# Optimization experiments

Hardware: AMD Instinct MI355X
Metric: run time of the kernel (lower is better)

The kernel has to match this reference:

```python
import jax, jax.numpy as jnp
import numpy as np

N_NODES = 100000
N_EDGES = 3200000
F_IN = 128
HID = 64
N_GRAPHS = 256
N_CLASSES = 8


def setup_inputs() -> dict:
    key = jax.random.key(0)
    ks = jax.random.split(key, 8)
    x = jax.random.normal(ks[0], (N_NODES, F_IN), dtype=jnp.float32)
    edge_index = jax.random.randint(ks[1], (2, N_EDGES), 0, N_NODES, dtype=jnp.int64)
    batch = jnp.sort(jax.random.randint(ks[2], (N_NODES,), 0, N_GRAPHS, dtype=jnp.int64))
    def glorot(k, fan_in, fan_out):
        s = np.sqrt(6.0 / (fan_in + fan_out)).astype(np.float32)
        return jax.random.uniform(k, (fan_in, fan_out), jnp.float32, -s, s)
    return {
        "x": x,
        "edge_index": edge_index,
        "batch": batch,
        "W1": glorot(ks[3], F_IN, HID),
        "b1": jnp.zeros((HID,), jnp.float32),
        "W2": glorot(ks[4], HID, HID),
        "b2": jnp.zeros((HID,), jnp.float32),
        "Wf1": glorot(ks[5], HID, 32),
        "bf1": jnp.zeros((32,), jnp.float32),
        "Wf2": glorot(ks[6], 32, N_CLASSES),
        "bf2": jnp.zeros((N_CLASSES,), jnp.float32),
    }


def gcn_conv(x, src, dst, dis, W, b, num_nodes):
    # PyG GCNConv: x' = D^{-1/2} (A + I) D^{-1/2} (x W) + b
    xw = x @ W  # [N, out]
    norm = dis[src] * dis[dst]  # [E+N] per-edge symmetric normalization
    out = jax.ops.segment_sum(norm[:, None] * xw[src], dst, num_segments=num_nodes)
    return out + b


def reference(x, edge_index, batch, W1, b1, W2, b2, Wf1, bf1, Wf2, bf2):
    n = x.shape[0]
    loop = jnp.arange(n, dtype=edge_index.dtype)
    src = jnp.concatenate([edge_index[0], loop])  # add self-loops (PyG default)
    dst = jnp.concatenate([edge_index[1], loop])
    deg = jax.ops.segment_sum(jnp.ones_like(dst, dtype=x.dtype), dst, num_segments=n)
    dis = jnp.where(deg > 0, jax.lax.rsqrt(jnp.maximum(deg, 1.0)), 0.0)

    h = jax.nn.relu(gcn_conv(x, src, dst, dis, W1, b1, n))
    h = gcn_conv(h, src, dst, dis, W2, b2, n)

    # global_mean_pool over graph segment ids
    sums = jax.ops.segment_sum(h, batch, num_segments=N_GRAPHS)  # [G, 64]
    counts = jax.ops.segment_sum(jnp.ones((n,), h.dtype), batch, num_segments=N_GRAPHS)
    pooled = sums / jnp.maximum(counts, 1.0)[:, None]

    out = jax.nn.relu(pooled @ Wf1 + bf1) @ Wf2 + bf2  # [G, num_classes]
    return out
```

## Files before the change

### kernel.cpp

```cpp
#include <hip/hip_runtime.h>
#include <hip/hip_bf16.h>


#define NGRAPHS 256

__device__ __forceinline__ float bflo(unsigned u) { return __uint_as_float(u << 16); }
__device__ __forceinline__ float bfhi(unsigned u) { return __uint_as_float(u & 0xffff0000u); }
__device__ __forceinline__ unsigned short bfpack1(float v) {
  unsigned ua = __float_as_uint(v);
  ua += 0x7fffu + ((ua >> 16) & 1u);
  return (unsigned short)(ua >> 16);
}
__device__ __forceinline__ unsigned bfpack2(float a, float b) {
  unsigned ua = __float_as_uint(a), ub = __float_as_uint(b);
  ua += 0x7fffu + ((ua >> 16) & 1u);
  ub += 0x7fffu + ((ub >> 16) & 1u);
  return (ua >> 16) | (ub & 0xffff0000u);
}

__global__ __launch_bounds__(256) void hist_kernel(const int* __restrict__ dst,
                                                   int* __restrict__ deg, int E) {
  int stride = gridDim.x * 256;
  for (int e = blockIdx.x * 256 + threadIdx.x; e < E; e += stride)
    atomicAdd(&deg[dst[e]], 1);
}

__global__ __launch_bounds__(256) void scan1_kernel(const int* __restrict__ deg,
                                                    int* __restrict__ bsum, int N) {
  __shared__ int red[4];
  int t = threadIdx.x;
  int base = blockIdx.x * 1024;
  int s = 0;
  for (int i = t; i < 1024; i += 256) {
    int idx = base + i;
    if (idx < N) s += deg[idx];
  }
#pragma unroll
  for (int o = 32; o > 0; o >>= 1) s += __shfl_down(s, o);
  if ((t & 63) == 0) red[t >> 6] = s;
  __syncthreads();
  if (t == 0) bsum[blockIdx.x] = red[0] + red[1] + red[2] + red[3];
}

__global__ __launch_bounds__(64) void scan2_kernel(int* __restrict__ bsum, int nb) {
  int lane = threadIdx.x;
  int v0 = lane < nb ? bsum[lane] : 0;
  int v1 = (64 + lane) < nb ? bsum[64 + lane] : 0;
  int x0 = v0, x1 = v1;
#pragma unroll
  for (int o = 1; o < 64; o <<= 1) {
    int y = __shfl_up(x0, o);
    if (lane >= o) x0 += y;
  }
#pragma unroll
  for (int o = 1; o < 64; o <<= 1) {
    int y = __shfl_up(x1, o);
    if (lane >= o) x1 += y;
  }
  int tot0 = __shfl(x0, 63);
  if (lane < nb) bsum[lane] = x0 - v0;
  if ((64 + lane) < nb) bsum[64 + lane] = tot0 + x1 - v1;
}

__global__ __launch_bounds__(256) void scan3_kernel(const int* __restrict__ deg,
                                                    const int* __restrict__ bsum,
                                                    int* __restrict__ offs,
                                                    float* __restrict__ dis, int N) {
  __shared__ int wtot[4];
  int t = threadIdx.x, lane = t & 63, w = t >> 6;
  int base = blockIdx.x * 1024 + t * 4;
  int d0 = (base + 0) < N ? deg[base + 0] : 0;
  int d1 = (base + 1) < N ? deg[base + 1] : 0;
  int d2 = (base + 2) < N ? deg[base + 2] : 0;
  int d3 = (base + 3) < N ? deg[base + 3] : 0;
  int ts = d0 + d1 + d2 + d3;
  int x = ts;
#pragma unroll
  for (int o = 1; o < 64; o <<= 1) {
    int y = __shfl_up(x, o);
    if (lane >= o) x += y;
  }
  if (lane == 63) wtot[w] = x;
  __syncthreads();
  int woff = 0;
  for (int i = 0; i < w; ++i) woff += wtot[i];
  int o0 = bsum[blockIdx.x] + woff + (x - ts);
  int o1 = o0 + d0, o2 = o1 + d1, o3 = o2 + d2;
  if (base + 0 < N) { offs[base + 0] = o0; dis[base + 0] = rsqrtf((float)(d0 + 1)); }
  if (base + 1 < N) { offs[base + 1] = o1; dis[base + 1] = rsqrtf((float)(d1 + 1)); }
  if (base + 2 < N) { offs[base + 2] = o2; dis[base + 2] = rsqrtf((float)(d2 + 1)); }
  if (base + 3 < N) { offs[base + 3] = o3; dis[base + 3] = rsqrtf((float)(d3 + 1)); }
  if (base + 0 == N - 1) offs[N] = o0 + d0;
  if (base + 1 == N - 1) offs[N] = o1 + d1;
  if (base + 2 == N - 1) offs[N] = o2 + d2;
  if (base + 3 == N - 1) offs[N] = o3 + d3;
}

__global__ __launch_bounds__(256) void fill_kernel(const int* __restrict__ src,
                                                   const int* __restrict__ dst,
                                                   const int* __restrict__ offs,
                                                   int* __restrict__ cur,
                                                   int* __restrict__ edata, int E) {
  int stride = gridDim.x * 256;
  for (int e = blockIdx.x * 256 + threadIdx.x; e < E; e += stride) {
    int d = dst[e];
    int pos = offs[d] + atomicAdd(&cur[d], 1);
    edata[pos] = src[e];
  }
}

__global__ __launch_bounds__(256) void gemm1_kernel(const float* __restrict__ X,
                                                    const float* __restrict__ W,
                                                    const float* __restrict__ dis,
                                                    unsigned short* __restrict__ Y,
                                                    int nrows) {
  __shared__ float ws[128][64];
  __shared__ float xs[16][128];
  int t = threadIdx.x;

  const float4* W4 = (const float4*)W;
  float4* ws4 = (float4*)(&ws[0][0]);
  for (int i = t; i < 128 * 64 / 4; i += 256) ws4[i] = W4[i];

  int row0 = blockIdx.x * 16;
  int nr = min(16, nrows - row0);
  const float4* X4 = (const float4*)(X + (size_t)row0 * 128);
  float4* xs4 = (float4*)(&xs[0][0]);
  for (int i = t; i < nr * 128 / 4; i += 256) xs4[i] = X4[i];
  __syncthreads();

  int wave = t >> 6, lane = t & 63;
  for (int r = wave; r < nr; r += 4) {
    float acc = 0.f;
#pragma unroll
    for (int k = 0; k < 128; k += 4) {
      acc += xs[r][k + 0] * ws[k + 0][lane];
      acc += xs[r][k + 1] * ws[k + 1][lane];
      acc += xs[r][k + 2] * ws[k + 2][lane];
      acc += xs[r][k + 3] * ws[k + 3][lane];
    }
    Y[(size_t)(row0 + r) * 64 + lane] = bfpack1(acc * dis[row0 + r]);
  }
}

__global__ __launch_bounds__(256) void gemm2_kernel(const unsigned* __restrict__ X32,
                                                    const float* __restrict__ W,
                                                    const float* __restrict__ dis,
                                                    unsigned short* __restrict__ Y,
                                                    int nrows) {
  __shared__ float ws[64][64];
  __shared__ unsigned xs[16][32];
  int t = threadIdx.x;

  const float4* W4 = (const float4*)W;
  float4* ws4 = (float4*)(&ws[0][0]);
  for (int i = t; i < 64 * 64 / 4; i += 256) ws4[i] = W4[i];

  int row0 = blockIdx.x * 16;
  int nr = min(16, nrows - row0);
  const uint4* X4 = (const uint4*)(X32 + (size_t)row0 * 32);
  uint4* xs4 = (uint4*)(&xs[0][0]);
  for (int i = t; i < nr * 32 / 4; i += 256) xs4[i] = X4[i];
  __syncthreads();

  int wave = t >> 6, lane = t & 63;
  for (int r = wave; r < nr; r += 4) {
    float acc = 0.f;
#pragma unroll
    for (int k2 = 0; k2 < 32; ++k2) {
      unsigned u = xs[r][k2];
      acc += bflo(u) * ws[2 * k2 + 0][lane];
      acc += bfhi(u) * ws[2 * k2 + 1][lane];
    }
    Y[(size_t)(row0 + r) * 64 + lane] = bfpack1(acc * dis[row0 + r]);
  }
}

template <bool POOL>
__global__ __launch_bounds__(256) void gather_kernel(const int* __restrict__ edata,
                                                     const int* __restrict__ offs,
                                                     const float* __restrict__ dis,
                                                     const unsigned* __restrict__ xw32,
                                                     const float* __restrict__ bias,
                                                     const int* __restrict__ batch,
                                                     unsigned* __restrict__ out32,
                                                     float* __restrict__ psum,
                                                     float* __restrict__ pcnt, int N) {
  int lane = threadIdx.x & 63;
  int half = lane >> 5;
  int f2 = lane & 31;
  int node = blockIdx.x * 4 + (threadIdx.x >> 6);
  if (node >= N) return;
  int beg = offs[node], end = offs[node + 1];
  float acc0 = 0.f, acc1 = 0.f;

  int j = beg;
  for (; j < end && (j & 3); ++j) {
    unsigned u = xw32[edata[j] * 32 + f2];
    if (half == 0) { acc0 += bflo(u); acc1 += bfhi(u); }
  }
  for (; j + 8 <= end; j += 8) {
    int4 a = *(const int4*)(edata + j);
    int4 b = *(const int4*)(edata + j + 4);
    int e0 = half ? a.y : a.x;
    int e1 = half ? a.w : a.z;
    int e2 = half ? b.y : b.x;
    int e3 = half ? b.w : b.z;
    unsigned u0 = xw32[e0 * 32 + f2];
    unsigned u1 = xw32[e1 * 32 + f2];
    unsigned u2 = xw32[e2 * 32 + f2];
    unsigned u3 = xw32[e3 * 32 + f2];
    acc0 += bflo(u0); acc1 += bfhi(u0);
    acc0 += bflo(u1); acc1 += bfhi(u1);
    acc0 += bflo(u2); acc1 += bfhi(u2);
    acc0 += bflo(u3); acc1 += bfhi(u3);
  }
  for (; j < end; ++j) {
    unsigned u = xw32[edata[j] * 32 + f2];
    if (half == 0) { acc0 += bflo(u); acc1 += bfhi(u); }
  }

  acc0 += __shfl_xor(acc0, 32);
  acc1 += __shfl_xor(acc1, 32);

  unsigned us = xw32[node * 32 + f2];
  acc0 += bflo(us);
  acc1 += bfhi(us);
  float d = dis[node];
  acc0 = fmaf(d, acc0, bias[2 * f2 + 0]);
  acc1 = fmaf(d, acc1, bias[2 * f2 + 1]);

  if (POOL) {
    if (half == 0) {
      int g = batch[node];
      atomicAdd(&psum[g * 64 + 2 * f2 + 0], acc0);
      atomicAdd(&psum[g * 64 + 2 * f2 + 1], acc1);
      if (f2 == 0) atomicAdd(&pcnt[g], 1.0f);
    }
  } else {
    if (half == 0)
      out32[node * 32 + f2] = bfpack2(fmaxf(acc0, 0.f), fmaxf(acc1, 0.f));
  }
}

__global__ __launch_bounds__(64) void mlp_kernel(const float* __restrict__ psum,
                                                 const float* __restrict__ pcnt,
                                                 const float* __restrict__ Wf1,
                                                 const float* __restrict__ bf1,
                                                 const float* __restrict__ Wf2,
                                                 const float* __restrict__ bf2,
                                                 float* __restrict__ out) {
  int g = blockIdx.x;
  int lane = threadIdx.x;
  __shared__ float p[64];
  __shared__ float hh[32];
  float cnt = fmaxf(pcnt[g], 1.f);
  p[lane] = psum[g * 64 + lane] / cnt;
  __syncthreads();
  if (lane < 32) {
    float a = bf1[lane];
#pragma unroll
    for (int f = 0; f < 64; ++f) a += p[f] * Wf1[f * 32 + lane];
    hh[lane] = fmaxf(a, 0.f);
  }
  __syncthreads();
  if (lane < 8) {
    float a = bf2[lane];
#pragma unroll
    for (int j = 0; j < 32; ++j) a += hh[j] * Wf2[j * 8 + lane];
    out[g * 8 + lane] = a;
  }
}

extern "C" void kernel_launch(void* const* d_in, const int* in_sizes, int n_in,
                              void* d_out, int out_size, void* d_ws, size_t ws_size,
                              hipStream_t stream) {
  const float* x     = (const float*)d_in[0];
  const int*   ei    = (const int*)d_in[1];
  const int*   batch = (const int*)d_in[2];
  const float* W1  = (const float*)d_in[3];
  const float* b1  = (const float*)d_in[4];
  const float* W2  = (const float*)d_in[5];
  const float* b2  = (const float*)d_in[6];
  const float* Wf1 = (const float*)d_in[7];
  const float* bf1 = (const float*)d_in[8];
  const float* Wf2 = (const float*)d_in[9];
  const float* bf2 = (const float*)d_in[10];
  float* out = (float*)d_out;

  const int N = in_sizes[0] / 128;
  const int E = in_sizes[1] / 2;
  const int* src = ei;
  const int* dst = ei + E;
  const int nb = (N + 1023) / 1024;

  int*      edata = (int*)d_ws;
  unsigned* xwA   = (unsigned*)(edata + E);
  unsigned* hB    = xwA + (size_t)N * 32;
  float*    dis   = (float*)(hB + (size_t)N * 32);
  int*      deg   = (int*)(dis + N);
  int*      offs  = deg + N;
  int*      cur   = offs + N + 1;
  int*      bsum  = cur + N;
  float*    psum  = (float*)(bsum + 128);
  float*    pcnt  = psum + NGRAPHS * 64;

  hipMemsetAsync(deg, 0, (size_t)N * sizeof(int), stream);
  hipMemsetAsync(cur, 0, (size_t)N * sizeof(int), stream);
  hist_kernel<<<2048, 256, 0, stream>>>(dst, deg, E);
  scan1_kernel<<<nb, 256, 0, stream>>>(deg, bsum, N);
  scan2_kernel<<<1, 64, 0, stream>>>(bsum, nb);
  scan3_kernel<<<nb, 256, 0, stream>>>(deg, bsum, offs, dis, N);
  fill_kernel<<<2048, 256, 0, stream>>>(src, dst, offs, cur, edata, E);

  gemm1_kernel<<<(N + 15) / 16, 256, 0, stream>>>(x, W1, dis, (unsigned short*)xwA, N);
  gather_kernel<false><<<(N + 3) / 4, 256, 0, stream>>>(edata, offs, dis, xwA, b1,
                                                        batch, hB, psum, pcnt, N);

  gemm2_kernel<<<(N + 15) / 16, 256, 0, stream>>>(hB, W2, dis, (unsigned short*)xwA, N);
  hipMemsetAsync(psum, 0, (NGRAPHS * 64 + NGRAPHS) * sizeof(float), stream);
  gather_kernel<true><<<(N + 3) / 4, 256, 0, stream>>>(edata, offs, dis, xwA, b2,
                                                       batch, hB, psum, pcnt, N);

  mlp_kernel<<<NGRAPHS, 64, 0, stream>>>(psum, pcnt, Wf1, bf1, Wf2, bf2, out);
}
```

Measured before the change: 1.059 ms.

## Gather with 16-byte row loads, eight edges per wave, software-prefetched indices

Reworks the neighbour-aggregation kernel so each wave processes eight edges per iteration. Each group of 8 lanes loads a full 128-byte bf16 row with 16-byte loads, replacing two edges per step with 4-byte loads. The next batch of edge indices is loaded before the current rows are accumulated, overlapping index fetches with row accumulation. Partial sums are combined across lane groups with a three-step shuffle reduction over 8 accumulators, which raises register use and shuffle count.

```diff
diff --git a/kernel.cpp b/kernel.cpp
--- a/kernel.cpp
+++ b/kernel.cpp
@@ -176,70 +176,103 @@
   }
 }
 
+__device__ __forceinline__ int select8(const int4& a, const int4& b, int sel) {
+  int4 c;
+  c.x = (sel & 4) ? b.x : a.x;
+  c.y = (sel & 4) ? b.y : a.y;
+  c.z = (sel & 4) ? b.z : a.z;
+  c.w = (sel & 4) ? b.w : a.w;
+  int lo = (sel & 1) ? c.y : c.x;
+  int hi = (sel & 1) ? c.w : c.z;
+  return (sel & 2) ? hi : lo;
+}
+
+__device__ __forceinline__ void accum8(float* acc, uint4 u) {
+  acc[0] += bflo(u.x); acc[1] += bfhi(u.x);
+  acc[2] += bflo(u.y); acc[3] += bfhi(u.y);
+  acc[4] += bflo(u.z); acc[5] += bfhi(u.z);
+  acc[6] += bflo(u.w); acc[7] += bfhi(u.w);
+}
+
 template <bool POOL>
 __global__ __launch_bounds__(256) void gather_kernel(const int* __restrict__ edata,
                                                      const int* __restrict__ offs,
                                                      const float* __restrict__ dis,
-                                                     const unsigned* __restrict__ xw32,
+                                                     const uint4* __restrict__ xw4,
                                                      const float* __restrict__ bias,
                                                      const int* __restrict__ batch,
-                                                     unsigned* __restrict__ out32,
+                                                     uint4* __restrict__ out4,
                                                      float* __restrict__ psum,
                                                      float* __restrict__ pcnt, int N) {
   int lane = threadIdx.x & 63;
-  int half = lane >> 5;
-  int f2 = lane & 31;
+  int sel = lane >> 3;
+  int fb = lane & 7;
   int node = blockIdx.x * 4 + (threadIdx.x >> 6);
   if (node >= N) return;
   int beg = offs[node], end = offs[node + 1];
-  float acc0 = 0.f, acc1 = 0.f;
+  float acc[8] = {0.f, 0.f, 0.f, 0.f, 0.f, 0.f, 0.f, 0.f};
 
   int j = beg;
   for (; j < end && (j & 3); ++j) {
-    unsigned u = xw32[edata[j] * 32 + f2];
-    if (half == 0) { acc0 += bflo(u); acc1 += bfhi(u); }
-  }
-  for (; j + 8 <= end; j += 8) {
-    int4 a = *(const int4*)(edata + j);
-    int4 b = *(const int4*)(edata + j + 4);
-    int e0 = half ? a.y : a.x;
-    int e1 = half ? a.w : a.z;
-    int e2 = half ? b.y : b.x;
-    int e3 = half ? b.w : b.z;
-    unsigned u0 = xw32[e0 * 32 + f2];
-    unsigned u1 = xw32[e1 * 32 + f2];
-    unsigned u2 = xw32[e2 * 32 + f2];
-    unsigned u3 = xw32[e3 * 32 + f2];
-    acc0 += bflo(u0); acc1 += bfhi(u0);
-    acc0 += bflo(u1); acc1 += bfhi(u1);
-    acc0 += bflo(u2); acc1 += bfhi(u2);
-    acc0 += bflo(u3); acc1 += bfhi(u3);
+    uint4 u = xw4[(size_t)edata[j] * 8 + fb];
+    if (sel == 0) accum8(acc, u);
+  }
+  int nfull = (end - j) >> 3;
+  if (nfull > 0) {
+    const int4* ep = (const int4*)(edata + j);
+    int4 a = ep[0], b = ep[1];
+    int g = 0;
+    for (;;) {
+      int idx = select8(a, b, sel);
+      uint4 u = xw4[(size_t)idx * 8 + fb];
+      ++g;
+      if (g >= nfull) { accum8(acc, u); break; }
+      a = ep[2 * g];
+      b = ep[2 * g + 1];
+      accum8(acc, u);
+    }
+    j += nfull * 8;
   }
   for (; j < end; ++j) {
-    unsigned u = xw32[edata[j] * 32 + f2];
-    if (half == 0) { acc0 += bflo(u); acc1 += bfhi(u); }
-  }
-
-  acc0 += __shfl_xor(acc0, 32);
-  acc1 += __shfl_xor(acc1, 32);
-
-  unsigned us = xw32[node * 32 + f2];
-  acc0 += bflo(us);
-  acc1 += bfhi(us);
+    uint4 u = xw4[(size_t)edata[j] * 8 + fb];
+    if (sel == 0) accum8(acc, u);
+  }
+
+#pragma unroll
+  for (int m = 8; m <= 32; m <<= 1) {
+#pragma unroll
+    for (int k = 0; k < 8; ++k) acc[k] += __shfl_xor(acc[k], m);
+  }
+
+  accum8(acc, xw4[(size_t)node * 8 + fb]);
+
   float d = dis[node];
-  acc0 = fmaf(d, acc0, bias[2 * f2 + 0]);
-  acc1 = fmaf(d, acc1, bias[2 * f2 + 1]);
+  float4 b0 = ((const float4*)bias)[fb * 2];
+  float4 b1 = ((const float4*)bias)[fb * 2 + 1];
+  float r0 = fmaf(d, acc[0], b0.x), r1 = fmaf(d, acc[1], b0.y);
+  float r2 = fmaf(d, acc[2], b0.z), r3 = fmaf(d, acc[3], b0.w);
+  float r4 = fmaf(d, acc[4], b1.x), r5 = fmaf(d, acc[5], b1.y);
+  float r6 = fmaf(d, acc[6], b1.z), r7 = fmaf(d, acc[7], b1.w);
 
   if (POOL) {
-    if (half == 0) {
+    if (sel == 0) {
       int g = batch[node];
-      atomicAdd(&psum[g * 64 + 2 * f2 + 0], acc0);
-      atomicAdd(&psum[g * 64 + 2 * f2 + 1], acc1);
-      if (f2 == 0) atomicAdd(&pcnt[g], 1.0f);
+      float* p = &psum[g * 64 + fb * 8];
+      atomicAdd(p + 0, r0); atomicAdd(p + 1, r1);
+      atomicAdd(p + 2, r2); atomicAdd(p + 3, r3);
+      atomicAdd(p + 4, r4); atomicAdd(p + 5, r5);
+      atomicAdd(p + 6, r6); atomicAdd(p + 7, r7);
+      if (fb == 0) atomicAdd(&pcnt[g], 1.0f);
     }
   } else {
-    if (half == 0)
-      out32[node * 32 + f2] = bfpack2(fmaxf(acc0, 0.f), fmaxf(acc1, 0.f));
+    if (sel == 0) {
+      uint4 o;
+      o.x = bfpack2(fmaxf(r0, 0.f), fmaxf(r1, 0.f));
+      o.y = bfpack2(fmaxf(r2, 0.f), fmaxf(r3, 0.f));
+      o.z = bfpack2(fmaxf(r4, 0.f), fmaxf(r5, 0.f));
+      o.w = bfpack2(fmaxf(r6, 0.f), fmaxf(r7, 0.f));
+      out4[(size_t)node * 8 + fb] = o;
+    }
   }
 }
 
@@ -314,13 +347,13 @@
   fill_kernel<<<2048, 256, 0, stream>>>(src, dst, offs, cur, edata, E);
 
   gemm1_kernel<<<(N + 15) / 16, 256, 0, stream>>>(x, W1, dis, (unsigned short*)xwA, N);
-  gather_kernel<false><<<(N + 3) / 4, 256, 0, stream>>>(edata, offs, dis, xwA, b1,
-                                                        batch, hB, psum, pcnt, N);
+  gather_kernel<false><<<(N + 3) / 4, 256, 0, stream>>>(edata, offs, dis, (const uint4*)xwA,
+                                                        b1, batch, (uint4*)hB, psum, pcnt, N);
 
   gemm2_kernel<<<(N + 15) / 16, 256, 0, stream>>>(hB, W2, dis, (unsigned short*)xwA, N);
   hipMemsetAsync(psum, 0, (NGRAPHS * 64 + NGRAPHS) * sizeof(float), stream);
-  gather_kernel<true><<<(N + 3) / 4, 256, 0, stream>>>(edata, offs, dis, xwA, b2,
-                                                       batch, hB, psum, pcnt, N);
+  gather_kernel<true><<<(N + 3) / 4, 256, 0, stream>>>(edata, offs, dis, (const uint4*)xwA,
+                                                       b2, batch, (uint4*)hB, psum, pcnt, N);
 
   mlp_kernel<<<NGRAPHS, 64, 0, stream>>>(psum, pcnt, Wf1, bf1, Wf2, bf2, out);
 }
```

Result: slower. 1.251 ms (+18.2%).

## Split each node's edge gather across two wavefronts with shared-memory reduction

Applied to the files above, without the earlier changes.

The gather kernel now assigns two wavefronts per destination node instead of one. Each wave processes alternating 8-edge groups, with the next group's indices software-prefetched. The partial sums are combined through shared memory after a block barrier. This doubles memory-level parallelism per node to hide the random-gather latency, at the cost of a __syncthreads, extra LDS traffic, twice as many blocks, and idle waves on low-degree nodes.

```diff
diff --git a/kernel.cpp b/kernel.cpp
--- a/kernel.cpp
+++ b/kernel.cpp
@@ -186,60 +186,85 @@
                                                      unsigned* __restrict__ out32,
                                                      float* __restrict__ psum,
                                                      float* __restrict__ pcnt, int N) {
-  int lane = threadIdx.x & 63;
+  __shared__ float part[4][2][32];
+  int tid = threadIdx.x;
+  int lane = tid & 63;
+  int wid = tid >> 6;
   int half = lane >> 5;
   int f2 = lane & 31;
-  int node = blockIdx.x * 4 + (threadIdx.x >> 6);
-  if (node >= N) return;
-  int beg = offs[node], end = offs[node + 1];
+  int node = blockIdx.x * 2 + (wid >> 1);
+  int sub = wid & 1;
   float acc0 = 0.f, acc1 = 0.f;
 
-  int j = beg;
-  for (; j < end && (j & 3); ++j) {
-    unsigned u = xw32[edata[j] * 32 + f2];
-    if (half == 0) { acc0 += bflo(u); acc1 += bfhi(u); }
-  }
-  for (; j + 8 <= end; j += 8) {
-    int4 a = *(const int4*)(edata + j);
-    int4 b = *(const int4*)(edata + j + 4);
-    int e0 = half ? a.y : a.x;
-    int e1 = half ? a.w : a.z;
-    int e2 = half ? b.y : b.x;
-    int e3 = half ? b.w : b.z;
-    unsigned u0 = xw32[e0 * 32 + f2];
-    unsigned u1 = xw32[e1 * 32 + f2];
-    unsigned u2 = xw32[e2 * 32 + f2];
-    unsigned u3 = xw32[e3 * 32 + f2];
-    acc0 += bflo(u0); acc1 += bfhi(u0);
-    acc0 += bflo(u1); acc1 += bfhi(u1);
-    acc0 += bflo(u2); acc1 += bfhi(u2);
-    acc0 += bflo(u3); acc1 += bfhi(u3);
-  }
-  for (; j < end; ++j) {
-    unsigned u = xw32[edata[j] * 32 + f2];
-    if (half == 0) { acc0 += bflo(u); acc1 += bfhi(u); }
+  int beg = 0, end = 0;
+  if (node < N) { beg = offs[node]; end = offs[node + 1]; }
+  int beg4 = min((beg + 3) & ~3, end);
+  int G = (end - beg4) >> 3;
+  int tail = beg4 + G * 8;
+
+  if (sub == 0) {
+    for (int j = beg; j < beg4; ++j) {
+      unsigned u = xw32[(size_t)edata[j] * 32 + f2];
+      if (half == 0) { acc0 += bflo(u); acc1 += bfhi(u); }
+    }
+  } else {
+    for (int j = tail; j < end; ++j) {
+      unsigned u = xw32[(size_t)edata[j] * 32 + f2];
+      if (half == 0) { acc0 += bflo(u); acc1 += bfhi(u); }
+    }
+  }
+
+  int g = sub;
+  if (g < G) {
+    const int4* ep = (const int4*)(edata + beg4);
+    int4 a = ep[2 * g], b = ep[2 * g + 1];
+    for (;;) {
+      int e0 = half ? a.y : a.x;
+      int e1 = half ? a.w : a.z;
+      int e2 = half ? b.y : b.x;
+      int e3 = half ? b.w : b.z;
+      unsigned u0 = xw32[(size_t)e0 * 32 + f2];
+      unsigned u1 = xw32[(size_t)e1 * 32 + f2];
+      unsigned u2 = xw32[(size_t)e2 * 32 + f2];
+      unsigned u3 = xw32[(size_t)e3 * 32 + f2];
+      int gn = g + 2;
+      bool more = gn < G;
+      int4 a2, b2;
+      if (more) { a2 = ep[2 * gn]; b2 = ep[2 * gn + 1]; }
+      acc0 += bflo(u0); acc1 += bfhi(u0);
+      acc0 += bflo(u1); acc1 += bfhi(u1);
+      acc0 += bflo(u2); acc1 += bfhi(u2);
+      acc0 += bflo(u3); acc1 += bfhi(u3);
+      if (!more) break;
+      a = a2; b = b2; g = gn;
+    }
   }
 
   acc0 += __shfl_xor(acc0, 32);
   acc1 += __shfl_xor(acc1, 32);
-
-  unsigned us = xw32[node * 32 + f2];
-  acc0 += bflo(us);
-  acc1 += bfhi(us);
-  float d = dis[node];
-  acc0 = fmaf(d, acc0, bias[2 * f2 + 0]);
-  acc1 = fmaf(d, acc1, bias[2 * f2 + 1]);
-
-  if (POOL) {
-    if (half == 0) {
-      int g = batch[node];
-      atomicAdd(&psum[g * 64 + 2 * f2 + 0], acc0);
-      atomicAdd(&psum[g * 64 + 2 * f2 + 1], acc1);
-      if (f2 == 0) atomicAdd(&pcnt[g], 1.0f);
-    }
-  } else {
-    if (half == 0)
-      out32[node * 32 + f2] = bfpack2(fmaxf(acc0, 0.f), fmaxf(acc1, 0.f));
+  if (half == 0) { part[wid][0][f2] = acc0; part[wid][1][f2] = acc1; }
+  __syncthreads();
+
+  if (node < N && sub == 0) {
+    acc0 += part[wid ^ 1][0][f2];
+    acc1 += part[wid ^ 1][1][f2];
+    unsigned us = xw32[(size_t)node * 32 + f2];
+    acc0 += bflo(us);
+    acc1 += bfhi(us);
+    float d = dis[node];
+    acc0 = fmaf(d, acc0, bias[2 * f2 + 0]);
+    acc1 = fmaf(d, acc1, bias[2 * f2 + 1]);
+    if (POOL) {
+      if (half == 0) {
+        int gb = batch[node];
+        atomicAdd(&psum[gb * 64 + 2 * f2 + 0], acc0);
+        atomicAdd(&psum[gb * 64 + 2 * f2 + 1], acc1);
+        if (f2 == 0) atomicAdd(&pcnt[gb], 1.0f);
+      }
+    } else {
+      if (half == 0)
+        out32[(size_t)node * 32 + f2] = bfpack2(fmaxf(acc0, 0.f), fmaxf(acc1, 0.f));
+    }
   }
 }
 
@@ -314,12 +339,12 @@
   fill_kernel<<<2048, 256, 0, stream>>>(src, dst, offs, cur, edata, E);
 
   gemm1_kernel<<<(N + 15) / 16, 256, 0, stream>>>(x, W1, dis, (unsigned short*)xwA, N);
-  gather_kernel<false><<<(N + 3) / 4, 256, 0, stream>>>(edata, offs, dis, xwA, b1,
+  gather_kernel<false><<<(N + 1) / 2, 256, 0, stream>>>(edata, offs, dis, xwA, b1,
                                                         batch, hB, psum, pcnt, N);
 
   gemm2_kernel<<<(N + 15) / 16, 256, 0, stream>>>(hB, W2, dis, (unsigned short*)xwA, N);
   hipMemsetAsync(psum, 0, (NGRAPHS * 64 + NGRAPHS) * sizeof(float), stream);
-  gather_kernel<true><<<(N + 3) / 4, 256, 0, stream>>>(edata, offs, dis, xwA, b2,
+  gather_kernel<true><<<(N + 1) / 2, 256, 0, stream>>>(edata, offs, dis, xwA, b2,
                                                        batch, hB, psum, pcnt, N);
 
   mlp_kernel<<<NGRAPHS, 64, 0, stream>>>(psum, pcnt, Wf1, bf1, Wf2, bf2, out);
```

Result: slower. 1.272 ms (+20.1%).
